# Optimization experiments

Hardware: AMD Instinct MI355X
Metric: run time of the kernel (lower is better)

Reference implementation:

```python
import jax, jax.numpy as jnp
import numpy as np

N_NODES = 1_000_000
N_EDGES = 16_000_000
D = 30            # num_feature hardcoded in the module
WINDOW = D // 6   # = 5
DEG_THRESH = 10
NUM_TYPES = 2


def setup_inputs() -> dict:
    key = jax.random.key(0)
    k1, k2, k3, k4 = jax.random.split(key, 4)
    x = jax.random.normal(k1, (N_NODES, D), dtype=jnp.float32)
    W = jax.random.normal(k2, (D, D), dtype=jnp.float32)
    edge_index = jax.random.randint(k3, (2, N_EDGES), 0, N_NODES, dtype=jnp.int64)
    atom_types = jax.random.randint(k4, (N_NODES,), 0, NUM_TYPES, dtype=jnp.int64)
    return {"x": x, "W": W, "edge_index": edge_index, "atom_types": atom_types}


def reference(x, W, edge_index, atom_types):
    n = x.shape[0]
    # --- degree count: torch.bincount(edge_index.reshape(-1)) ---
    flat = edge_index.reshape(-1)
    count = jnp.zeros((n,), jnp.int32).at[flat].add(1)
    crit_count = (count > DEG_THRESH).astype(jnp.int32)  # criterion_count

    # --- type-mixture scatter-min over edges ---
    src, dst = edge_index[0], edge_index[1]
    same = atom_types[src] == atom_types[dst]
    # edge contributes 0 if types differ, else type+1, to BOTH endpoints; take min
    val = jnp.where(same, atom_types[src].astype(jnp.int32) + 1, 0)
    BIG = jnp.iinfo(jnp.int32).max
    mix = jnp.full((n,), BIG, jnp.int32)
    mix = mix.at[src].min(val).at[dst].min(val)
    mix = jnp.where(mix == BIG, 0, mix)  # isolated atoms -> 0

    crit = crit_count * 3 + mix  # criterion in [0, 5]

    # --- windowed one-hot criterion matrix [n, D] ---
    cols = jnp.arange(D, dtype=jnp.int32)
    start = (crit * WINDOW)[:, None]
    mask = ((cols[None, :] >= start) & (cols[None, :] < start + WINDOW)).astype(x.dtype)

    # --- e3nn Linear (30x0e -> 30x0e): dense matmul with 1/sqrt(fan_in) path norm ---
    scale = np.float32(1.0 / np.sqrt(D))
    return (x @ W) * scale * mask
```

## Files before the change

### kernel.cpp

```cpp
#include <hip/hip_runtime.h>

#define N_NODES    1000000
#define N_EDGES    16000000
#define D          30
#define WINDOW     5
#define DEG_THRESH 10

#define P_PARTS    31
#define PART_BITS  15
#define PART_SIZE  32768
#define CAP        1081344
#define BUF_CAP    512
#define BIN_BLOCKS 256
#define BIN_THREADS 1024
#define BIN_ITERS  16
#define N_GROUPS   (N_EDGES / 4)
#define BM_WORDS   (N_NODES / 32)

#define L_BM_BYTES   125000
#define L_BUF_BYTES  (P_PARTS * BUF_CAP * 2)
#define L_CNT_OFF    (L_BM_BYTES + L_BUF_BYTES)
#define L_TOTAL      (L_CNT_OFF + P_PARTS * 4 * 3)

#define SLICES     8
#define HIST_WORDS 16384

#define WS_BM_OFF      0
#define WS_CUR_OFF     131072
#define WS_PART_OFF    131328
#define WS_NEEDED      (WS_PART_OFF + (size_t)P_PARTS * SLICES * HIST_WORDS * 4)
#define OUT_BYTES_NEEDED ((size_t)P_PARTS * CAP * 2)

__global__ __launch_bounds__(256) void pack_types(
    const int* __restrict__ types,
    unsigned*  __restrict__ bm,
    unsigned*  __restrict__ cursors)
{
    const int g = blockIdx.x * 256 + threadIdx.x;
    const int v = (g < N_NODES) ? types[g] : 0;
    const unsigned long long m = __ballot(v);
    if ((threadIdx.x & 31) == 0 && g < N_NODES)
        bm[g >> 5] = (unsigned)(m >> (threadIdx.x & 32));
    if (blockIdx.x == 0 && threadIdx.x < 64) cursors[threadIdx.x] = 0u;
}

__global__ __launch_bounds__(BIN_THREADS, 1) void bin_edges(
    const int*      __restrict__ edge_index,
    const unsigned* __restrict__ bm,
    unsigned short* __restrict__ buckets,
    unsigned*       __restrict__ cursors)
{
    extern __shared__ char smem[];
    unsigned* bm_lds = (unsigned*)smem;
    unsigned short (*buf)[BUF_CAP] =
        (unsigned short(*)[BUF_CAP])(smem + L_BM_BYTES);
    unsigned* cnt   = (unsigned*)(smem + L_CNT_OFF);
    unsigned* basev = cnt + P_PARTS;
    unsigned* ccnt  = basev + P_PARTS;

    const int tid = threadIdx.x;
    for (int i = tid; i < BM_WORDS; i += BIN_THREADS) bm_lds[i] = bm[i];
    if (tid < P_PARTS) cnt[tid] = 0u;
    __syncthreads();

    for (int it = 0; it < BIN_ITERS; ++it) {
        const int g = (blockIdx.x * BIN_ITERS + it) * BIN_THREADS + tid;
        if (g < N_GROUPS) {
            const int e0 = g * 4;
            const int4 s4 = *reinterpret_cast<const int4*>(edge_index + e0);
            const int4 d4 = *reinterpret_cast<const int4*>(edge_index + N_EDGES + e0);
            const int ss[4] = {s4.x, s4.y, s4.z, s4.w};
            const int dd[4] = {d4.x, d4.y, d4.z, d4.w};
#pragma unroll
            for (int k = 0; k < 4; ++k) {
                const int s = ss[k], d = dd[k];
                const unsigned ts = (bm_lds[(unsigned)s >> 5] >> (s & 31)) & 1u;
                const unsigned td = (bm_lds[(unsigned)d >> 5] >> (d & 31)) & 1u;
                {
                    const int b = s >> PART_BITS;
                    const unsigned short rec =
                        (unsigned short)(((s & (PART_SIZE - 1)) << 1) | td);
                    const unsigned pos = atomicAdd(&cnt[b], 1u);
                    if (pos < BUF_CAP) buf[b][pos] = rec;
                    else {
                        const unsigned gp = atomicAdd(&cursors[b], 1u);
                        if (gp < CAP) buckets[(size_t)b * CAP + gp] = rec;
                    }
                }
                {
                    const int b = d >> PART_BITS;
                    const unsigned short rec =
                        (unsigned short)(((d & (PART_SIZE - 1)) << 1) | ts);
                    const unsigned pos = atomicAdd(&cnt[b], 1u);
                    if (pos < BUF_CAP) buf[b][pos] = rec;
                    else {
                        const unsigned gp = atomicAdd(&cursors[b], 1u);
                        if (gp < CAP) buckets[(size_t)b * CAP + gp] = rec;
                    }
                }
            }
        }
        __syncthreads();
        if (tid < P_PARTS) {
            unsigned c = cnt[tid]; if (c > BUF_CAP) c = BUF_CAP;
            unsigned bse = 0u;
            if (c) {
                bse = atomicAdd(&cursors[tid], c);
                if (bse > CAP) bse = CAP;
                if (bse + c > CAP) c = CAP - bse;
            }
            ccnt[tid] = c; basev[tid] = bse; cnt[tid] = 0u;
        }
        __syncthreads();
        const int w = tid >> 6, lane = tid & 63;
#pragma unroll
        for (int j = 0; j < 2; ++j) {
            const int b = w * 2 + j;
            if (b < P_PARTS) {
                const unsigned c = ccnt[b];
                unsigned short* dst = buckets + (size_t)b * CAP + basev[b];
                for (unsigned e = lane; e < c; e += 64) dst[e] = buf[b][e];
            }
        }
        __syncthreads();
    }
}

__global__ __launch_bounds__(512) void hist_pass(
    const unsigned short* __restrict__ buckets,
    const unsigned*       __restrict__ cursors,
    unsigned*             __restrict__ partials)
{
    __shared__ unsigned hist[HIST_WORDS];
    const int p = blockIdx.x >> 3, s = blockIdx.x & 7;
    const int tid = threadIdx.x;
    for (int i = tid; i < HIST_WORDS; i += 512) hist[i] = 0u;
    __syncthreads();

    unsigned count = cursors[p]; if (count > CAP) count = CAP;
    const unsigned short* bk = buckets + (size_t)p * CAP;
    const unsigned n4 = (count + 3u) >> 2;
    for (unsigned j = (unsigned)(s * 512 + tid); j < n4; j += SLICES * 512) {
        const unsigned i0 = j * 4u;
        if (i0 + 4u <= count) {
            const ushort4 r4 = *reinterpret_cast<const ushort4*>(bk + i0);
            const unsigned short rr[4] = {r4.x, r4.y, r4.z, r4.w};
#pragma unroll
            for (int k = 0; k < 4; ++k) {
                const unsigned rec = rr[k];
                const unsigned local = rec >> 1, t = rec & 1u;
                atomicAdd(&hist[local >> 1], (1u << (8u * t)) << (16u * (local & 1u)));
            }
        } else {
            for (unsigned i = i0; i < count; ++i) {
                const unsigned rec = bk[i];
                const unsigned local = rec >> 1, t = rec & 1u;
                atomicAdd(&hist[local >> 1], (1u << (8u * t)) << (16u * (local & 1u)));
            }
        }
    }
    __syncthreads();
    unsigned* op = partials + (size_t)blockIdx.x * HIST_WORDS;
    for (int i = tid; i < HIST_WORDS; i += 512) op[i] = hist[i];
}

#define WT_STRIDE 36
__global__ __launch_bounds__(512) void out_pass(
    const float* __restrict__ x, const float* __restrict__ Wm,
    const unsigned* __restrict__ partials,
    const unsigned* __restrict__ bm,
    float* __restrict__ out)
{
    __shared__ float sWt[D * WT_STRIDE];
    const int tid = threadIdx.x;
    for (int i = tid; i < D * D; i += 512) {
        const int k = i / D, c = i - k * D;
        sWt[c * WT_STRIDE + k] = Wm[i];
    }
    __syncthreads();

    const long n = (long)blockIdx.x * 512 + tid;
    if (n >= N_NODES) return;

    const unsigned Wd   = (unsigned)(n >> 1);
    const unsigned h    = (unsigned)n & 1u;
    const unsigned p    = Wd >> 14;
    const unsigned widx = Wd & 16383u;
    const unsigned* pp  = partials + (size_t)(p * SLICES) * HIST_WORDS + widx;
    unsigned sum = 0u;
#pragma unroll
    for (int s = 0; s < SLICES; ++s) sum += pp[(size_t)s * HIST_WORDS];
    const unsigned c0 = (sum >> (16u * h)) & 0xFFu;
    const unsigned c1 = (sum >> (16u * h + 8u)) & 0xFFu;
    const unsigned t  = (bm[n >> 5] >> ((unsigned)n & 31u)) & 1u;
    const unsigned cnt    = c0 + c1;
    const unsigned same_c = t ? c1 : c0;
    const unsigned diff_c = t ? c0 : c1;
    const int mix  = diff_c ? 0 : (same_c ? (int)t + 1 : 0);
    const int crit = (cnt > DEG_THRESH ? 3 : 0) + mix;

    float xr[D];
    const float2* xb = reinterpret_cast<const float2*>(x + (size_t)n * D);
#pragma unroll
    for (int i = 0; i < D / 2; ++i) {
        const float2 v = xb[i];
        xr[2 * i] = v.x; xr[2 * i + 1] = v.y;
    }

    float acc[WINDOW];
    const float* wc0 = &sWt[(crit * WINDOW) * WT_STRIDE];
#pragma unroll
    for (int j = 0; j < WINDOW; ++j) {
        const float* wc = wc0 + j * WT_STRIDE;
        float a = 0.0f;
#pragma unroll
        for (int k = 0; k < D; ++k) a += xr[k] * wc[k];
        acc[j] = a * 0.18257418583505536f;
    }

    float2 o[D / 2];
#pragma unroll
    for (int q = 0; q < D / WINDOW; ++q) {
        const bool m = (q == crit);
#pragma unroll
        for (int r = 0; r < WINDOW; ++r) {
            const float v = m ? acc[r] : 0.0f;
            const int c = WINDOW * q + r;
            if (c & 1) o[c >> 1].y = v; else o[c >> 1].x = v;
        }
    }
    float2* ob = reinterpret_cast<float2*>(out + (size_t)n * D);
#pragma unroll
    for (int i = 0; i < D / 2; ++i) ob[i] = o[i];
}

#define SAME_INC (1u << 12)
#define DIFF_INC (1u << 22)

__global__ __launch_bounds__(256) void edge_pass_atomic(
    const int* __restrict__ edge_index, const int* __restrict__ atom_types,
    unsigned* __restrict__ agg)
{
    const int t  = blockIdx.x * blockDim.x + threadIdx.x;
    const int e0 = t * 4;
    if (e0 >= N_EDGES) return;
    const int4 s4 = *reinterpret_cast<const int4*>(edge_index + e0);
    const int4 d4 = *reinterpret_cast<const int4*>(edge_index + N_EDGES + e0);
    const int ss[4] = {s4.x, s4.y, s4.z, s4.w};
    const int dd[4] = {d4.x, d4.y, d4.z, d4.w};
#pragma unroll
    for (int k = 0; k < 4; ++k) {
        const int s = ss[k], d = dd[k];
        const unsigned add = 1u + ((atom_types[s] == atom_types[d]) ? SAME_INC : DIFF_INC);
        atomicAdd(agg + s, add);
        atomicAdd(agg + d, add);
    }
}

__global__ __launch_bounds__(256) void out_pass_agg(
    const float* __restrict__ x, const float* __restrict__ Wm,
    const unsigned* __restrict__ agg, const int* __restrict__ atom_types,
    float* __restrict__ out)
{
    __shared__ float sx[64 * D];
    __shared__ float sW[D * D];
    __shared__ int   sstart[64];
    const int tid   = threadIdx.x;
    const long base = (long)blockIdx.x * 64;
    for (int i = tid; i < D * D; i += 256) sW[i] = Wm[i];
    const float* xb = x + base * D;
    for (int i = tid; i < 64 * D; i += 256) sx[i] = xb[i];
    if (tid < 64) {
        const long n = base + tid;
        const unsigned a = agg[n];
        const int cnt = a & 0xFFFu, sc = (a >> 12) & 0x3FFu, dc = a >> 22;
        const int mix  = dc ? 0 : (sc ? atom_types[n] + 1 : 0);
        sstart[tid] = ((cnt > DEG_THRESH ? 3 : 0) + mix) * WINDOW;
    }
    __syncthreads();
    const float scale = 0.18257418583505536f;
    float* ob = out + base * D;
    for (int i = tid; i < 64 * D; i += 256) {
        const int nd = i / D, c = i - nd * D;
        float v = 0.0f;
        if ((unsigned)(c - sstart[nd]) < WINDOW) {
            float acc = 0.0f;
#pragma unroll
            for (int k = 0; k < D; ++k) acc += sx[nd * D + k] * sW[k * D + c];
            v = acc * scale;
        }
        ob[i] = v;
    }
}

extern "C" void kernel_launch(void* const* d_in, const int* in_sizes, int n_in,
                              void* d_out, int out_size, void* d_ws, size_t ws_size,
                              hipStream_t stream)
{
    const float* x          = (const float*)d_in[0];
    const float* Wm         = (const float*)d_in[1];
    const int*   edge_index = (const int*)d_in[2];
    const int*   atom_types = (const int*)d_in[3];
    float* out = (float*)d_out;

    if (ws_size >= WS_NEEDED && (size_t)out_size * 4 >= OUT_BYTES_NEEDED) {
        char* ws = (char*)d_ws;
        unsigned*       bm       = (unsigned*)(ws + WS_BM_OFF);
        unsigned*       cursors  = (unsigned*)(ws + WS_CUR_OFF);
        unsigned*       partials = (unsigned*)(ws + WS_PART_OFF);
        unsigned short* buckets  = (unsigned short*)d_out;

        pack_types<<<(N_NODES + 255) / 256, 256, 0, stream>>>(atom_types, bm, cursors);
        bin_edges<<<BIN_BLOCKS, BIN_THREADS, L_TOTAL, stream>>>(edge_index, bm,
                                                                buckets, cursors);
        hist_pass<<<P_PARTS * SLICES, 512, 0, stream>>>(buckets, cursors, partials);
        out_pass<<<(N_NODES + 511) / 512, 512, 0, stream>>>(
            x, Wm, partials, bm, out);
    } else {
        unsigned* agg = (unsigned*)d_ws;
        hipMemsetAsync(agg, 0x00, N_NODES * sizeof(unsigned), stream);
        edge_pass_atomic<<<(N_EDGES / 4) / 256, 256, 0, stream>>>(edge_index, atom_types, agg);
        out_pass_agg<<<N_NODES / 64, 256, 0, stream>>>(x, Wm, agg, atom_types, out);
    }
}
```

Measured before the change: 395.6 us.

## Stage x and output rows through LDS for coalesced global access in out_pass

The output kernel now loads each wave's 64 rows of x through a padded shared-memory staging tile with fully coalesced float2 reads, and writes the output back the same way instead of using per-thread strided row accesses. Block size drops from 512 to 256 threads to fit the staging buffer. The aim is fewer uncoalesced memory transactions on the 120 MB x read and the 120 MB output write. In exchange it adds extra LDS traffic and block barriers, and the reduced occupancy may hurt latency hiding. The hist_pass store loop bound also changes to a literal 512*32, which is only equivalent if HIST_WORDS equals that value.

```diff
diff --git a/kernel.cpp b/kernel.cpp
--- a/kernel.cpp
+++ b/kernel.cpp
@@ -161,54 +161,73 @@
     }
     __syncthreads();
     unsigned* op = partials + (size_t)blockIdx.x * HIST_WORDS;
-    for (int i = tid; i < HIST_WORDS; i += 512) op[i] = hist[i];
-}
-
-#define WT_STRIDE 36
-__global__ __launch_bounds__(512) void out_pass(
+    for (int i = tid; i < 512 * 32; i += 512) op[i] = hist[i];
+}
+
+#define WT_STRIDE  36
+#define OT_THREADS 256
+#define OT_ROWPAD  33
+__global__ __launch_bounds__(OT_THREADS) void out_pass(
     const float* __restrict__ x, const float* __restrict__ Wm,
     const unsigned* __restrict__ partials,
     const unsigned* __restrict__ bm,
     float* __restrict__ out)
 {
     __shared__ float sWt[D * WT_STRIDE];
+    __shared__ float stg[OT_THREADS / 64][64 * OT_ROWPAD];
     const int tid = threadIdx.x;
-    for (int i = tid; i < D * D; i += 512) {
+    for (int i = tid; i < D * D; i += OT_THREADS) {
         const int k = i / D, c = i - k * D;
         sWt[c * WT_STRIDE + k] = Wm[i];
     }
-    __syncthreads();
-
-    const long n = (long)blockIdx.x * 512 + tid;
-    if (n >= N_NODES) return;
-
-    const unsigned Wd   = (unsigned)(n >> 1);
-    const unsigned h    = (unsigned)n & 1u;
-    const unsigned p    = Wd >> 14;
-    const unsigned widx = Wd & 16383u;
-    const unsigned* pp  = partials + (size_t)(p * SLICES) * HIST_WORDS + widx;
-    unsigned sum = 0u;
-#pragma unroll
-    for (int s = 0; s < SLICES; ++s) sum += pp[(size_t)s * HIST_WORDS];
-    const unsigned c0 = (sum >> (16u * h)) & 0xFFu;
-    const unsigned c1 = (sum >> (16u * h + 8u)) & 0xFFu;
-    const unsigned t  = (bm[n >> 5] >> ((unsigned)n & 31u)) & 1u;
-    const unsigned cnt    = c0 + c1;
-    const unsigned same_c = t ? c1 : c0;
-    const unsigned diff_c = t ? c0 : c1;
-    const int mix  = diff_c ? 0 : (same_c ? (int)t + 1 : 0);
-    const int crit = (cnt > DEG_THRESH ? 3 : 0) + mix;
+
+    const int wv = tid >> 6, lane = tid & 63;
+    const long blockBase = (long)blockIdx.x * OT_THREADS;
+    const long waveBase  = blockBase + (long)wv * 64;
+    float* ws = stg[wv];
+    const long f2base = waveBase * 15;
+    const long f2lim  = (long)N_NODES * 15;
+
+    const float2* gx = reinterpret_cast<const float2*>(x);
+#pragma unroll
+    for (int it = 0; it < 15; ++it) {
+        const int g = it * 64 + lane;
+        const int row = g / 15, c2 = g - row * 15;
+        float2 v = make_float2(0.0f, 0.0f);
+        if (f2base + g < f2lim) v = gx[f2base + g];
+        ws[row * OT_ROWPAD + 2 * c2]     = v.x;
+        ws[row * OT_ROWPAD + 2 * c2 + 1] = v.y;
+    }
+    __syncthreads();
+
+    const long n = blockBase + tid;
+    int start = 0;
+    if (n < N_NODES) {
+        const unsigned Wd   = (unsigned)(n >> 1);
+        const unsigned h    = (unsigned)n & 1u;
+        const unsigned p    = Wd >> 14;
+        const unsigned widx = Wd & 16383u;
+        const unsigned* pp  = partials + (size_t)(p * SLICES) * HIST_WORDS + widx;
+        unsigned sum = 0u;
+#pragma unroll
+        for (int s = 0; s < SLICES; ++s) sum += pp[(size_t)s * HIST_WORDS];
+        const unsigned c0 = (sum >> (16u * h)) & 0xFFu;
+        const unsigned c1 = (sum >> (16u * h + 8u)) & 0xFFu;
+        const unsigned t  = (bm[n >> 5] >> ((unsigned)n & 31u)) & 1u;
+        const unsigned cnt    = c0 + c1;
+        const unsigned same_c = t ? c1 : c0;
+        const unsigned diff_c = t ? c0 : c1;
+        const int mix  = diff_c ? 0 : (same_c ? (int)t + 1 : 0);
+        const int crit = (cnt > DEG_THRESH ? 3 : 0) + mix;
+        start = crit * WINDOW;
+    }
 
     float xr[D];
-    const float2* xb = reinterpret_cast<const float2*>(x + (size_t)n * D);
-#pragma unroll
-    for (int i = 0; i < D / 2; ++i) {
-        const float2 v = xb[i];
-        xr[2 * i] = v.x; xr[2 * i + 1] = v.y;
-    }
+#pragma unroll
+    for (int k = 0; k < D; ++k) xr[k] = ws[lane * OT_ROWPAD + k];
 
     float acc[WINDOW];
-    const float* wc0 = &sWt[(crit * WINDOW) * WT_STRIDE];
+    const float* wc0 = &sWt[start * WT_STRIDE];
 #pragma unroll
     for (int j = 0; j < WINDOW; ++j) {
         const float* wc = wc0 + j * WT_STRIDE;
@@ -217,21 +236,24 @@
         for (int k = 0; k < D; ++k) a += xr[k] * wc[k];
         acc[j] = a * 0.18257418583505536f;
     }
-
-    float2 o[D / 2];
-#pragma unroll
-    for (int q = 0; q < D / WINDOW; ++q) {
-        const bool m = (q == crit);
-#pragma unroll
-        for (int r = 0; r < WINDOW; ++r) {
-            const float v = m ? acc[r] : 0.0f;
-            const int c = WINDOW * q + r;
-            if (c & 1) o[c >> 1].y = v; else o[c >> 1].x = v;
-        }
-    }
-    float2* ob = reinterpret_cast<float2*>(out + (size_t)n * D);
-#pragma unroll
-    for (int i = 0; i < D / 2; ++i) ob[i] = o[i];
+    __syncthreads();
+
+    float* wr = ws + lane * OT_ROWPAD;
+#pragma unroll
+    for (int k = 0; k < D; ++k) wr[k] = 0.0f;
+#pragma unroll
+    for (int j = 0; j < WINDOW; ++j) wr[start + j] = acc[j];
+    __syncthreads();
+
+    float2* gout = reinterpret_cast<float2*>(out);
+#pragma unroll
+    for (int it = 0; it < 15; ++it) {
+        const int g = it * 64 + lane;
+        const int row = g / 15, c2 = g - row * 15;
+        if (f2base + g < f2lim)
+            gout[f2base + g] = make_float2(ws[row * OT_ROWPAD + 2 * c2],
+                                           ws[row * OT_ROWPAD + 2 * c2 + 1]);
+    }
 }
 
 #define SAME_INC (1u << 12)
@@ -314,7 +336,7 @@
         bin_edges<<<BIN_BLOCKS, BIN_THREADS, L_TOTAL, stream>>>(edge_index, bm,
                                                                 buckets, cursors);
         hist_pass<<<P_PARTS * SLICES, 512, 0, stream>>>(buckets, cursors, partials);
-        out_pass<<<(N_NODES + 511) / 512, 512, 0, stream>>>(
+        out_pass<<<(N_NODES + OT_THREADS - 1) / OT_THREADS, OT_THREADS, 0, stream>>>(
             x, Wm, partials, bm, out);
     } else {
         unsigned* agg = (unsigned*)d_ws;
```

After: 384.1 us. 2.9% less time.
